# Kernel tuning notes

Measured on AMD Instinct MI355X. Metric: run time of the kernel, lower is better.

Reference implementation:

```python
import jax, jax.numpy as jnp
import numpy as np
from jax import lax


def setup_inputs() -> dict:
    key = jax.random.key(0)
    k1, k2, k3 = jax.random.split(key, 3)
    B, P, D = 4, 64, 768
    N, R = 2048, 12
    positions = jax.random.normal(k1, (B, P, D), dtype=jnp.float32)
    # module inits keys with std=0.01 (we use randn*0.01); adjacency is a learned
    # dense R x N x N parameter (init zeros in source -> use small noise so the
    # read path is non-degenerate for kernel correctness checks)
    keys_param = jax.random.normal(k2, (N, D), dtype=jnp.float32) * 0.01
    adjacency = jax.random.normal(k3, (R, N, N), dtype=jnp.float32) * 0.01
    return {"positions": positions, "keys_param": keys_param,
            "adjacency": adjacency, "k": 16}


def reference(positions, keys_param, adjacency, k):
    # keys property: L2-normalize along feature dim
    keys = keys_param * lax.rsqrt(
        jnp.sum(keys_param * keys_param, axis=-1, keepdims=True) + 1e-12)

    # anchor: key matching scores = positions . keys^T  -> (B, P, N)
    scores = jnp.einsum('bpd,nd->bpn', positions, keys)

    # topk_sparse addressing: keep top-k nodes per position, normalize to sum 1
    vals, idx = lax.top_k(scores, k)           # (B, P, k)
    w = jax.nn.softmax(vals, axis=-1)          # normalized anchor weights

    # read: position -> node -> (rel, nei_node), honoring top-k sparsity by
    # gathering only the k selected adjacency rows per relation (no dense BPN matmul)
    adj_rows = adjacency[:, idx, :]            # (R, B, P, k, N) gather
    nei = jnp.einsum('bpk,rbpkn->bpn', w, adj_rows)   # neighbor node scores

    # project neighbor node distribution back through keys -> (B, P, D)
    out = jnp.einsum('bpn,nd->bpd', nei, keys)
    return out
```

## Files before the change

kernel.cpp:

```cpp
#include <hip/hip_runtime.h>
#include <math.h>

#define B_ 4
#define P_ 64
#define D_ 768
#define N_ 2048
#define R_ 12
#define K_ 16
#define Q_ 256
#define SPLITS_ 8
#define BK_ 32
#define NEG_INF_ -3.0e38f

__global__ __launch_bounds__(256) void k_norm(const float* __restrict__ kp,
                                              float* __restrict__ keys) {
    int row = blockIdx.x;
    int tid = threadIdx.x;
    const float* src = kp + (size_t)row * D_;
    float x0 = src[tid], x1 = src[tid + 256], x2 = src[tid + 512];
    float ss = x0 * x0 + x1 * x1 + x2 * x2;
    #pragma unroll
    for (int off = 32; off > 0; off >>= 1) ss += __shfl_down(ss, off, 64);
    __shared__ float sm[4];
    if ((tid & 63) == 0) sm[tid >> 6] = ss;
    __syncthreads();
    float tot = sm[0] + sm[1] + sm[2] + sm[3];
    float inv = 1.0f / sqrtf(tot + 1e-12f);
    float* dst = keys + (size_t)row * D_;
    dst[tid] = x0 * inv;
    dst[tid + 256] = x1 * inv;
    dst[tid + 512] = x2 * inv;
}

__global__ __launch_bounds__(256) void k_scores(const float* __restrict__ pos,
                                                const float* __restrict__ keys,
                                                float* __restrict__ spart) {
    __shared__ float Ast[BK_][68];
    __shared__ float Bst[BK_][68];
    int tid = threadIdx.x;
    int tx = tid & 15, ty = tid >> 4;
    int n0 = blockIdx.x * 64, q0 = blockIdx.y * 64;
    int z = blockIdx.z;
    float acc[4][4] = {};
    for (int kb = z * (D_ / 2); kb < (z + 1) * (D_ / 2); kb += BK_) {
        #pragma unroll
        for (int e = 0; e < 2; e++) {
            int elem = tid + e * 256;
            int row = elem >> 3, c4 = elem & 7;
            float4 v = *(const float4*)(pos + (size_t)(q0 + row) * D_ + kb + c4 * 4);
            Ast[c4 * 4 + 0][row] = v.x; Ast[c4 * 4 + 1][row] = v.y;
            Ast[c4 * 4 + 2][row] = v.z; Ast[c4 * 4 + 3][row] = v.w;
        }
        #pragma unroll
        for (int e = 0; e < 2; e++) {
            int elem = tid + e * 256;
            int row = elem >> 3, c4 = elem & 7;
            float4 v = *(const float4*)(keys + (size_t)(n0 + row) * D_ + kb + c4 * 4);
            Bst[c4 * 4 + 0][row] = v.x; Bst[c4 * 4 + 1][row] = v.y;
            Bst[c4 * 4 + 2][row] = v.z; Bst[c4 * 4 + 3][row] = v.w;
        }
        __syncthreads();
        #pragma unroll 4
        for (int kk = 0; kk < BK_; kk++) {
            float4 a = *(const float4*)&Ast[kk][ty * 4];
            float4 b = *(const float4*)&Bst[kk][tx * 4];
            float av[4] = {a.x, a.y, a.z, a.w};
            float bv[4] = {b.x, b.y, b.z, b.w};
            #pragma unroll
            for (int i = 0; i < 4; i++)
                #pragma unroll
                for (int j = 0; j < 4; j++)
                    acc[i][j] += av[i] * bv[j];
        }
        __syncthreads();
    }
    float* base = spart + (size_t)z * Q_ * N_;
    #pragma unroll
    for (int i = 0; i < 4; i++) {
        float4 v = {acc[i][0], acc[i][1], acc[i][2], acc[i][3]};
        *(float4*)(base + (size_t)(q0 + ty * 4 + i) * N_ + n0 + tx * 4) = v;
    }
}

__global__ __launch_bounds__(256) void k_topk(const float* __restrict__ s0,
                                              const float* __restrict__ s1,
                                              float* __restrict__ wout,
                                              int* __restrict__ iout) {
    int q = blockIdx.x, tid = threadIdx.x;
    int w = tid >> 6, lane = tid & 63;
    int base = w * 512 + lane;
    const float* r0 = s0 + (size_t)q * N_;
    const float* r1 = s1 + (size_t)q * N_;
    float v[8];
    #pragma unroll
    for (int j = 0; j < 8; j++) {
        int n = base + j * 64;
        v[j] = r0[n] + r1[n];
    }
    __shared__ float cv[64];
    __shared__ int ci[64];
    for (int r = 0; r < K_; r++) {
        float bv = NEG_INF_;
        int bi = 0;
        #pragma unroll
        for (int j = 0; j < 8; j++) {
            int n = base + j * 64;
            if (v[j] > bv) { bv = v[j]; bi = n; }
        }
        #pragma unroll
        for (int off = 1; off < 64; off <<= 1) {
            float ov = __shfl_xor(bv, off, 64);
            int oi = __shfl_xor(bi, off, 64);
            if (ov > bv || (ov == bv && oi < bi)) { bv = ov; bi = oi; }
        }
        if (lane == 0) { cv[w * K_ + r] = bv; ci[w * K_ + r] = bi; }
        #pragma unroll
        for (int j = 0; j < 8; j++)
            if (base + j * 64 == bi) v[j] = NEG_INF_;
    }
    __syncthreads();
    if (w == 0) {
        float mv = cv[lane];
        int mi = ci[lane];
        float sel_v = NEG_INF_;
        int sel_i = 0;
        for (int r = 0; r < K_; r++) {
            float bv = mv;
            int bi = mi;
            #pragma unroll
            for (int off = 1; off < 64; off <<= 1) {
                float ov = __shfl_xor(bv, off, 64);
                int oi = __shfl_xor(bi, off, 64);
                if (ov > bv || (ov == bv && oi < bi)) { bv = ov; bi = oi; }
            }
            if (lane == r) { sel_v = bv; sel_i = bi; }
            if (mi == bi) mv = NEG_INF_;
        }
        float m = __shfl(sel_v, 0, 64);
        float e = (lane < K_) ? expf(sel_v - m) : 0.0f;
        float sum = e;
        #pragma unroll
        for (int off = 1; off < 64; off <<= 1) sum += __shfl_xor(sum, off, 64);
        if (lane < K_) {
            wout[q * K_ + lane] = e / sum;
            iout[q * K_ + lane] = sel_i;
        }
    }
}

__global__ __launch_bounds__(256) void k_asum(const float* __restrict__ adj,
                                              float* __restrict__ asum) {
    size_t i = (size_t)blockIdx.x * 256 + threadIdx.x;
    const float4* a4 = (const float4*)adj;
    const size_t plane = (size_t)N_ * N_ / 4;
    float4 acc = {0.f, 0.f, 0.f, 0.f};
    #pragma unroll
    for (int r = 0; r < R_; r++) {
        float4 v = a4[(size_t)r * plane + i];
        acc.x += v.x; acc.y += v.y; acc.z += v.z; acc.w += v.w;
    }
    ((float4*)asum)[i] = acc;
}

__global__ __launch_bounds__(256) void k_nei(const float* __restrict__ asum,
                                             const float* __restrict__ wv,
                                             const int* __restrict__ iv,
                                             float* __restrict__ nei) {
    int q = blockIdx.x, tid = threadIdx.x;
    __shared__ float wi[K_];
    __shared__ int ii[K_];
    if (tid < K_) { wi[tid] = wv[q * K_ + tid]; ii[tid] = iv[q * K_ + tid]; }
    __syncthreads();
    float4 acc0 = {0.f, 0.f, 0.f, 0.f};
    float4 acc1 = {0.f, 0.f, 0.f, 0.f};
    #pragma unroll
    for (int k = 0; k < K_; k++) {
        const float4* row = (const float4*)(asum + (size_t)ii[k] * N_);
        float wk = wi[k];
        float4 v0 = row[tid], v1 = row[tid + 256];
        acc0.x += wk * v0.x; acc0.y += wk * v0.y; acc0.z += wk * v0.z; acc0.w += wk * v0.w;
        acc1.x += wk * v1.x; acc1.y += wk * v1.y; acc1.z += wk * v1.z; acc1.w += wk * v1.w;
    }
    float4* dst = (float4*)(nei + (size_t)q * N_);
    dst[tid] = acc0;
    dst[tid + 256] = acc1;
}

__global__ __launch_bounds__(256) void k_out_part(const float* __restrict__ nei,
                                                  const float* __restrict__ keys,
                                                  float* __restrict__ part) {
    __shared__ float Ast[BK_][68];
    __shared__ float Bst[BK_][68];
    int tid = threadIdx.x;
    int tx = tid & 15, ty = tid >> 4;
    int d0 = blockIdx.x * 64;
    int q0 = blockIdx.y * 64;
    int z = blockIdx.z;
    float acc[4][4] = {};
    for (int kb = z * (N_ / SPLITS_); kb < (z + 1) * (N_ / SPLITS_); kb += BK_) {
        #pragma unroll
        for (int e = 0; e < 2; e++) {
            int elem = tid + e * 256;
            int row = elem >> 3, c4 = elem & 7;
            float4 v = *(const float4*)(nei + (size_t)(q0 + row) * N_ + kb + c4 * 4);
            Ast[c4 * 4 + 0][row] = v.x; Ast[c4 * 4 + 1][row] = v.y;
            Ast[c4 * 4 + 2][row] = v.z; Ast[c4 * 4 + 3][row] = v.w;
        }
        #pragma unroll
        for (int e = 0; e < 2; e++) {
            int elem = tid + e * 256;
            int kr = elem >> 4, c4 = elem & 15;
            float4 v = *(const float4*)(keys + (size_t)(kb + kr) * D_ + d0 + c4 * 4);
            *(float4*)&Bst[kr][c4 * 4] = v;
        }
        __syncthreads();
        #pragma unroll 4
        for (int kk = 0; kk < BK_; kk++) {
            float4 a = *(const float4*)&Ast[kk][ty * 4];
            float4 b = *(const float4*)&Bst[kk][tx * 4];
            float av[4] = {a.x, a.y, a.z, a.w};
            float bv[4] = {b.x, b.y, b.z, b.w};
            #pragma unroll
            for (int i = 0; i < 4; i++)
                #pragma unroll
                for (int j = 0; j < 4; j++)
                    acc[i][j] += av[i] * bv[j];
        }
        __syncthreads();
    }
    float* base = part + (size_t)z * Q_ * D_;
    #pragma unroll
    for (int i = 0; i < 4; i++) {
        float4 v = {acc[i][0], acc[i][1], acc[i][2], acc[i][3]};
        *(float4*)(base + (size_t)(q0 + ty * 4 + i) * D_ + d0 + tx * 4) = v;
    }
}

__global__ __launch_bounds__(256) void k_reduce(const float* __restrict__ part,
                                                float* __restrict__ out) {
    int i = blockIdx.x * 256 + threadIdx.x;
    const float4* p4 = (const float4*)part;
    const int plane = Q_ * D_ / 4;
    float4 acc = {0.f, 0.f, 0.f, 0.f};
    #pragma unroll
    for (int z = 0; z < SPLITS_; z++) {
        float4 v = p4[(size_t)z * plane + i];
        acc.x += v.x; acc.y += v.y; acc.z += v.z; acc.w += v.w;
    }
    ((float4*)out)[i] = acc;
}

extern "C" void kernel_launch(void* const* d_in, const int* in_sizes, int n_in,
                              void* d_out, int out_size, void* d_ws, size_t ws_size,
                              hipStream_t stream) {
    const float* pos = (const float*)d_in[0];
    const float* kp  = (const float*)d_in[1];
    const float* adj = (const float*)d_in[2];
    float* out = (float*)d_out;

    float* ws     = (float*)d_ws;
    float* keys   = ws;
    float* asum   = keys + (size_t)N_ * D_;
    float* spart  = asum + (size_t)N_ * N_;
    float* nei    = spart + 2 * (size_t)Q_ * N_;
    float* wbuf   = nei + (size_t)Q_ * N_;
    int*   ibuf   = (int*)(wbuf + Q_ * K_);
    float* part   = asum;

    k_norm<<<N_, 256, 0, stream>>>(kp, keys);
    k_scores<<<dim3(32, 4, 2), 256, 0, stream>>>(pos, keys, spart);
    k_topk<<<Q_, 256, 0, stream>>>(spart, spart + (size_t)Q_ * N_, wbuf, ibuf);
    k_asum<<<4096, 256, 0, stream>>>(adj, asum);
    k_nei<<<Q_, 256, 0, stream>>>(asum, wbuf, ibuf, nei);
    k_out_part<<<dim3(12, 4, SPLITS_), 256, 0, stream>>>(nei, keys, part);
    k_reduce<<<192, 256, 0, stream>>>(part, out);
}
```

Baseline: 387.4 us.

## Fuse norm, scores and adjacency sum into one launch; fold topk with nei

Merges key normalization, the score GEMM and the adjacency relation-sum into a single heterogeneous kernel. The score GEMM now runs on raw keys and applies per-key inverse norms inside top-k, which removes the dependency on normalized keys. Top-k and the neighbor gather are fused so weights and indices stay in shared memory. The K-split for scores rises to 4 and the output split count to 16. The goal is fewer launches and more parallel work for the memory-bound adjacency sum, at the cost of more partial-sum traffic.

New measurement: 340.5 us. 12.1% less time.

```diff
diff --git a/kernel.cpp b/kernel.cpp
--- a/kernel.cpp
+++ b/kernel.cpp
@@ -8,97 +8,117 @@
 #define R_ 12
 #define K_ 16
 #define Q_ 256
-#define SPLITS_ 8
+#define SSPLIT_ 4
+#define SPLITS_ 16
 #define BK_ 32
 #define NEG_INF_ -3.0e38f
 
-__global__ __launch_bounds__(256) void k_norm(const float* __restrict__ kp,
-                                              float* __restrict__ keys) {
-    int row = blockIdx.x;
-    int tid = threadIdx.x;
-    const float* src = kp + (size_t)row * D_;
-    float x0 = src[tid], x1 = src[tid + 256], x2 = src[tid + 512];
-    float ss = x0 * x0 + x1 * x1 + x2 * x2;
-    #pragma unroll
-    for (int off = 32; off > 0; off >>= 1) ss += __shfl_down(ss, off, 64);
-    __shared__ float sm[4];
-    if ((tid & 63) == 0) sm[tid >> 6] = ss;
-    __syncthreads();
-    float tot = sm[0] + sm[1] + sm[2] + sm[3];
-    float inv = 1.0f / sqrtf(tot + 1e-12f);
-    float* dst = keys + (size_t)row * D_;
-    dst[tid] = x0 * inv;
-    dst[tid + 256] = x1 * inv;
-    dst[tid + 512] = x2 * inv;
-}
-
-__global__ __launch_bounds__(256) void k_scores(const float* __restrict__ pos,
-                                                const float* __restrict__ keys,
-                                                float* __restrict__ spart) {
+__global__ __launch_bounds__(256) void k_front(const float* __restrict__ pos,
+                                               const float* __restrict__ kp,
+                                               const float* __restrict__ adj,
+                                               float* __restrict__ spart,
+                                               float* __restrict__ keys,
+                                               float* __restrict__ invn,
+                                               float* __restrict__ asum) {
     __shared__ float Ast[BK_][68];
     __shared__ float Bst[BK_][68];
+    int bid = blockIdx.x;
     int tid = threadIdx.x;
-    int tx = tid & 15, ty = tid >> 4;
-    int n0 = blockIdx.x * 64, q0 = blockIdx.y * 64;
-    int z = blockIdx.z;
-    float acc[4][4] = {};
-    for (int kb = z * (D_ / 2); kb < (z + 1) * (D_ / 2); kb += BK_) {
-        #pragma unroll
-        for (int e = 0; e < 2; e++) {
-            int elem = tid + e * 256;
-            int row = elem >> 3, c4 = elem & 7;
-            float4 v = *(const float4*)(pos + (size_t)(q0 + row) * D_ + kb + c4 * 4);
-            Ast[c4 * 4 + 0][row] = v.x; Ast[c4 * 4 + 1][row] = v.y;
-            Ast[c4 * 4 + 2][row] = v.z; Ast[c4 * 4 + 3][row] = v.w;
-        }
-        #pragma unroll
-        for (int e = 0; e < 2; e++) {
-            int elem = tid + e * 256;
-            int row = elem >> 3, c4 = elem & 7;
-            float4 v = *(const float4*)(keys + (size_t)(n0 + row) * D_ + kb + c4 * 4);
-            Bst[c4 * 4 + 0][row] = v.x; Bst[c4 * 4 + 1][row] = v.y;
-            Bst[c4 * 4 + 2][row] = v.z; Bst[c4 * 4 + 3][row] = v.w;
-        }
-        __syncthreads();
-        #pragma unroll 4
-        for (int kk = 0; kk < BK_; kk++) {
-            float4 a = *(const float4*)&Ast[kk][ty * 4];
-            float4 b = *(const float4*)&Bst[kk][tx * 4];
-            float av[4] = {a.x, a.y, a.z, a.w};
-            float bv[4] = {b.x, b.y, b.z, b.w};
-            #pragma unroll
-            for (int i = 0; i < 4; i++)
+    if (bid < 512) {
+        int z = bid >> 7;
+        int t = bid & 127;
+        int n0 = (t & 31) * 64, q0 = (t >> 5) * 64;
+        int tx = tid & 15, ty = tid >> 4;
+        float acc[4][4] = {};
+        for (int kb = z * (D_ / SSPLIT_); kb < (z + 1) * (D_ / SSPLIT_); kb += BK_) {
+            #pragma unroll
+            for (int e = 0; e < 2; e++) {
+                int elem = tid + e * 256;
+                int row = elem >> 3, c4 = elem & 7;
+                float4 v = *(const float4*)(pos + (size_t)(q0 + row) * D_ + kb + c4 * 4);
+                Ast[c4 * 4 + 0][row] = v.x; Ast[c4 * 4 + 1][row] = v.y;
+                Ast[c4 * 4 + 2][row] = v.z; Ast[c4 * 4 + 3][row] = v.w;
+            }
+            #pragma unroll
+            for (int e = 0; e < 2; e++) {
+                int elem = tid + e * 256;
+                int row = elem >> 3, c4 = elem & 7;
+                float4 v = *(const float4*)(kp + (size_t)(n0 + row) * D_ + kb + c4 * 4);
+                Bst[c4 * 4 + 0][row] = v.x; Bst[c4 * 4 + 1][row] = v.y;
+                Bst[c4 * 4 + 2][row] = v.z; Bst[c4 * 4 + 3][row] = v.w;
+            }
+            __syncthreads();
+            #pragma unroll 4
+            for (int kk = 0; kk < BK_; kk++) {
+                float4 a = *(const float4*)&Ast[kk][ty * 4];
+                float4 b = *(const float4*)&Bst[kk][tx * 4];
+                float av[4] = {a.x, a.y, a.z, a.w};
+                float bv[4] = {b.x, b.y, b.z, b.w};
                 #pragma unroll
-                for (int j = 0; j < 4; j++)
-                    acc[i][j] += av[i] * bv[j];
-        }
-        __syncthreads();
-    }
-    float* base = spart + (size_t)z * Q_ * N_;
-    #pragma unroll
-    for (int i = 0; i < 4; i++) {
-        float4 v = {acc[i][0], acc[i][1], acc[i][2], acc[i][3]};
-        *(float4*)(base + (size_t)(q0 + ty * 4 + i) * N_ + n0 + tx * 4) = v;
-    }
-}
-
-__global__ __launch_bounds__(256) void k_topk(const float* __restrict__ s0,
-                                              const float* __restrict__ s1,
-                                              float* __restrict__ wout,
-                                              int* __restrict__ iout) {
+                for (int i = 0; i < 4; i++)
+                    #pragma unroll
+                    for (int j = 0; j < 4; j++)
+                        acc[i][j] += av[i] * bv[j];
+            }
+            __syncthreads();
+        }
+        float* base = spart + (size_t)z * Q_ * N_;
+        #pragma unroll
+        for (int i = 0; i < 4; i++) {
+            float4 v = {acc[i][0], acc[i][1], acc[i][2], acc[i][3]};
+            *(float4*)(base + (size_t)(q0 + ty * 4 + i) * N_ + n0 + tx * 4) = v;
+        }
+    } else if (bid < 1024) {
+        int row = (bid - 512) * 4 + (tid >> 6);
+        int lane = tid & 63;
+        const float4* src = (const float4*)(kp + (size_t)row * D_);
+        float4 a = src[lane], b = src[lane + 64], c = src[lane + 128];
+        float ss = a.x * a.x + a.y * a.y + a.z * a.z + a.w * a.w
+                 + b.x * b.x + b.y * b.y + b.z * b.z + b.w * b.w
+                 + c.x * c.x + c.y * c.y + c.z * c.z + c.w * c.w;
+        #pragma unroll
+        for (int off = 32; off > 0; off >>= 1) ss += __shfl_down(ss, off, 64);
+        ss = __shfl(ss, 0, 64);
+        float inv = 1.0f / sqrtf(ss + 1e-12f);
+        float4* dst = (float4*)(keys + (size_t)row * D_);
+        float4 oa = {a.x * inv, a.y * inv, a.z * inv, a.w * inv};
+        float4 ob = {b.x * inv, b.y * inv, b.z * inv, b.w * inv};
+        float4 oc = {c.x * inv, c.y * inv, c.z * inv, c.w * inv};
+        dst[lane] = oa; dst[lane + 64] = ob; dst[lane + 128] = oc;
+        if (lane == 0) invn[row] = inv;
+    } else {
+        size_t i = (size_t)(bid - 1024) * 256 + tid;
+        const float4* a4 = (const float4*)adj;
+        const size_t plane = (size_t)N_ * N_ / 4;
+        float4 acc = {0.f, 0.f, 0.f, 0.f};
+        #pragma unroll
+        for (int r = 0; r < R_; r++) {
+            float4 v = a4[(size_t)r * plane + i];
+            acc.x += v.x; acc.y += v.y; acc.z += v.z; acc.w += v.w;
+        }
+        ((float4*)asum)[i] = acc;
+    }
+}
+
+__global__ __launch_bounds__(256) void k_topk_nei(const float* __restrict__ spart,
+                                                  const float* __restrict__ invn,
+                                                  const float* __restrict__ asum,
+                                                  float* __restrict__ nei) {
     int q = blockIdx.x, tid = threadIdx.x;
     int w = tid >> 6, lane = tid & 63;
     int base = w * 512 + lane;
-    const float* r0 = s0 + (size_t)q * N_;
-    const float* r1 = s1 + (size_t)q * N_;
+    const float* r0 = spart + (size_t)q * N_;
+    const size_t pl = (size_t)Q_ * N_;
     float v[8];
     #pragma unroll
     for (int j = 0; j < 8; j++) {
         int n = base + j * 64;
-        v[j] = r0[n] + r1[n];
+        v[j] = (r0[n] + r0[pl + n] + r0[2 * pl + n] + r0[3 * pl + n]) * invn[n];
     }
     __shared__ float cv[64];
     __shared__ int ci[64];
+    __shared__ float sw[K_];
+    __shared__ int si[K_];
     for (int r = 0; r < K_; r++) {
         float bv = NEG_INF_;
         int bi = 0;
@@ -141,42 +161,15 @@
         float sum = e;
         #pragma unroll
         for (int off = 1; off < 64; off <<= 1) sum += __shfl_xor(sum, off, 64);
-        if (lane < K_) {
-            wout[q * K_ + lane] = e / sum;
-            iout[q * K_ + lane] = sel_i;
-        }
-    }
-}
-
-__global__ __launch_bounds__(256) void k_asum(const float* __restrict__ adj,
-                                              float* __restrict__ asum) {
-    size_t i = (size_t)blockIdx.x * 256 + threadIdx.x;
-    const float4* a4 = (const float4*)adj;
-    const size_t plane = (size_t)N_ * N_ / 4;
-    float4 acc = {0.f, 0.f, 0.f, 0.f};
-    #pragma unroll
-    for (int r = 0; r < R_; r++) {
-        float4 v = a4[(size_t)r * plane + i];
-        acc.x += v.x; acc.y += v.y; acc.z += v.z; acc.w += v.w;
-    }
-    ((float4*)asum)[i] = acc;
-}
-
-__global__ __launch_bounds__(256) void k_nei(const float* __restrict__ asum,
-                                             const float* __restrict__ wv,
-                                             const int* __restrict__ iv,
-                                             float* __restrict__ nei) {
-    int q = blockIdx.x, tid = threadIdx.x;
-    __shared__ float wi[K_];
-    __shared__ int ii[K_];
-    if (tid < K_) { wi[tid] = wv[q * K_ + tid]; ii[tid] = iv[q * K_ + tid]; }
+        if (lane < K_) { sw[lane] = e / sum; si[lane] = sel_i; }
+    }
     __syncthreads();
     float4 acc0 = {0.f, 0.f, 0.f, 0.f};
     float4 acc1 = {0.f, 0.f, 0.f, 0.f};
     #pragma unroll
     for (int k = 0; k < K_; k++) {
-        const float4* row = (const float4*)(asum + (size_t)ii[k] * N_);
-        float wk = wi[k];
+        const float4* row = (const float4*)(asum + (size_t)si[k] * N_);
+        float wk = sw[k];
         float4 v0 = row[tid], v1 = row[tid + 256];
         acc0.x += wk * v0.x; acc0.y += wk * v0.y; acc0.z += wk * v0.z; acc0.w += wk * v0.w;
         acc1.x += wk * v1.x; acc1.y += wk * v1.y; acc1.z += wk * v1.z; acc1.w += wk * v1.w;
@@ -260,18 +253,14 @@
 
     float* ws     = (float*)d_ws;
     float* keys   = ws;
-    float* asum   = keys + (size_t)N_ * D_;
+    float* invn   = keys + (size_t)N_ * D_;
+    float* asum   = invn + N_;
     float* spart  = asum + (size_t)N_ * N_;
-    float* nei    = spart + 2 * (size_t)Q_ * N_;
-    float* wbuf   = nei + (size_t)Q_ * N_;
-    int*   ibuf   = (int*)(wbuf + Q_ * K_);
+    float* nei    = spart + (size_t)SSPLIT_ * Q_ * N_;
     float* part   = asum;
 
-    k_norm<<<N_, 256, 0, stream>>>(kp, keys);
-    k_scores<<<dim3(32, 4, 2), 256, 0, stream>>>(pos, keys, spart);
-    k_topk<<<Q_, 256, 0, stream>>>(spart, spart + (size_t)Q_ * N_, wbuf, ibuf);
-    k_asum<<<4096, 256, 0, stream>>>(adj, asum);
-    k_nei<<<Q_, 256, 0, stream>>>(asum, wbuf, ibuf, nei);
+    k_front<<<5120, 256, 0, stream>>>(pos, kp, adj, spart, keys, invn, asum);
+    k_topk_nei<<<Q_, 256, 0, stream>>>(spart, invn, asum, nei);
     k_out_part<<<dim3(12, 4, SPLITS_), 256, 0, stream>>>(nei, keys, part);
     k_reduce<<<192, 256, 0, stream>>>(part, out);
 }
```
